# Kernel optimization log

Measured on AMD Instinct MI355X. Metric: run time of the kernel, lower is better.

## Reference

```python
import jax, jax.numpy as jnp
import numpy as np

GROUPS = 32
EPS = 1e-5
HEADS = 8
HEAD_DIM = 40
INNER = HEADS * HEAD_DIM  # 320
QUERY_DIM = 320
CONTEXT_DIM = 768


def setup_inputs() -> dict:
    key = jax.random.key(0)
    ks = jax.random.split(key, 9)
    B, C, H, W = 16, QUERY_DIM, 64, 64
    Lc = 77
    x = jax.random.normal(ks[0], (B, C, H, W), dtype=jnp.float32)
    context = jax.random.normal(ks[1], (B, Lc, CONTEXT_DIM), dtype=jnp.float32)
    # Linear weights in torch layout (out_features, in_features), no bias for q/k/v
    Wq = jax.random.normal(ks[2], (INNER, QUERY_DIM), dtype=jnp.float32) * (QUERY_DIM ** -0.5)
    Wk = jax.random.normal(ks[3], (INNER, CONTEXT_DIM), dtype=jnp.float32) * (CONTEXT_DIM ** -0.5)
    Wv = jax.random.normal(ks[4], (INNER, CONTEXT_DIM), dtype=jnp.float32) * (CONTEXT_DIM ** -0.5)
    Wo = jax.random.normal(ks[5], (QUERY_DIM, INNER), dtype=jnp.float32) * (INNER ** -0.5)
    bo = jnp.zeros((QUERY_DIM,), dtype=jnp.float32)
    gn_scale = jnp.ones((QUERY_DIM,), dtype=jnp.float32)
    gn_bias = jnp.zeros((QUERY_DIM,), dtype=jnp.float32)
    return {"x": x, "context": context, "Wq": Wq, "Wk": Wk, "Wv": Wv,
            "Wo": Wo, "bo": bo, "gn_scale": gn_scale, "gn_bias": gn_bias}


def _group_norm(x, scale, bias):
    # x: [B, C, H, W]
    B, C, H, W = x.shape
    xg = x.reshape(B, GROUPS, C // GROUPS, H, W)
    mean = jnp.mean(xg, axis=(2, 3, 4), keepdims=True)
    var = jnp.var(xg, axis=(2, 3, 4), keepdims=True)
    xn = ((xg - mean) * jax.lax.rsqrt(var + EPS)).reshape(B, C, H, W)
    return xn * scale[None, :, None, None] + bias[None, :, None, None]


def reference(x, context, Wq, Wk, Wv, Wo, bo, gn_scale, gn_bias):
    B, C, H, W = x.shape
    residual = x
    xn = _group_norm(x, gn_scale, gn_bias)
    # (B, C, H, W) -> (B, H*W, C)
    tokens = xn.reshape(B, C, H * W).transpose(0, 2, 1)
    S = H * W
    Lc = context.shape[1]
    scale = HEAD_DIM ** -0.5
    # projections (Linear: x @ W.T); split heads -> [B, h, S, d]
    q = jnp.einsum('bsc,ec->bse', tokens, Wq).reshape(B, S, HEADS, HEAD_DIM).transpose(0, 2, 1, 3)
    k = jnp.einsum('blc,ec->ble', context, Wk).reshape(B, Lc, HEADS, HEAD_DIM).transpose(0, 2, 1, 3)
    v = jnp.einsum('blc,ec->ble', context, Wv).reshape(B, Lc, HEADS, HEAD_DIM).transpose(0, 2, 1, 3)
    scores = jnp.einsum('bhsd,bhkd->bhsk', q, k) * scale  # [B, h, S, Lc]
    attn = jax.nn.softmax(scores, axis=-1)
    out = jnp.einsum('bhsk,bhkd->bhsd', attn, v)  # [B, h, S, d]
    out = out.transpose(0, 2, 1, 3).reshape(B, S, INNER)
    out = jnp.einsum('bse,ce->bsc', out, Wo) + bo  # to_out (dropout is identity at eval)
    out = out.transpose(0, 2, 1).reshape(B, C, H, W)
    return out + residual
```

## Files before the change

### kernel.cpp

```cpp
#include <hip/hip_runtime.h>
#include <hip/hip_bf16.h>
#include <stdint.h>

#define B_    16
#define C_    320
#define S_    4096
#define G_    32
#define LC    77
#define CTX   768
#define HEADS 8
#define HD    40

typedef __bf16 bf16x8_t __attribute__((ext_vector_type(8)));
typedef float  f32x4_t  __attribute__((ext_vector_type(4)));

__device__ __forceinline__ unsigned short f2bf(float f) {
    union { float f; unsigned int u; } v; v.f = f;
    unsigned int r = v.u + 0x7fffu + ((v.u >> 16) & 1u);
    return (unsigned short)(r >> 16);
}
__device__ __forceinline__ float bf2f(unsigned short h) {
    union { unsigned int u; float f; } v; v.u = ((unsigned int)h) << 16;
    return v.f;
}

__device__ __forceinline__ void gload16(const void* g, void* l) {
    __builtin_amdgcn_global_load_lds(
        (const __attribute__((address_space(1))) unsigned int*)g,
        (__attribute__((address_space(3))) unsigned int*)l, 16, 0, 0);
}

__global__ __launch_bounds__(256) void gn_stats(const float* __restrict__ x,
                                                float2* __restrict__ mr) {
    int bg = blockIdx.x;
    const float4* p = (const float4*)(x + (size_t)bg * 40960);
    float s = 0.f, s2 = 0.f;
    for (int i = threadIdx.x; i < 10240; i += 256) {
        float4 v = p[i];
        s  += v.x + v.y + v.z + v.w;
        s2 += v.x * v.x + v.y * v.y + v.z * v.z + v.w * v.w;
    }
    for (int o = 32; o; o >>= 1) {
        s  += __shfl_down(s, o);
        s2 += __shfl_down(s2, o);
    }
    __shared__ float2 red[4];
    int lane = threadIdx.x & 63, wid = threadIdx.x >> 6;
    if (lane == 0) red[wid] = make_float2(s, s2);
    __syncthreads();
    if (threadIdx.x == 0) {
        float a = 0.f, c = 0.f;
        for (int i = 0; i < 4; i++) { a += red[i].x; c += red[i].y; }
        float mean = a / 40960.f;
        float var  = c / 40960.f - mean * mean;
        mr[bg] = make_float2(mean, rsqrtf(var + 1e-5f));
    }
}

__global__ __launch_bounds__(256) void castw(const float* __restrict__ s,
                                             unsigned short* __restrict__ d) {
    int i = blockIdx.x * 256 + threadIdx.x;
    float4 v = ((const float4*)s)[i];
    ushort4 o;
    o.x = f2bf(v.x); o.y = f2bf(v.y); o.z = f2bf(v.z); o.w = f2bf(v.w);
    ((ushort4*)d)[i] = o;
}

__global__ __launch_bounds__(256) void norm_tr(const float* __restrict__ x,
                                               const float2* __restrict__ mr,
                                               const float* __restrict__ gns,
                                               const float* __restrict__ gnb,
                                               unsigned short* __restrict__ tok) {
    int s0 = blockIdx.x * 32, c0 = blockIdx.y * 32, b = blockIdx.z;
    __shared__ unsigned short t[32][33];
    int tx = threadIdx.x & 31, ty = threadIdx.x >> 5;
    #pragma unroll
    for (int i = 0; i < 4; i++) {
        int cl = i * 8 + ty;
        int c = c0 + cl;
        float2 m = mr[b * 32 + c / 10];
        float v = x[((size_t)(b * 320 + c)) * 4096 + s0 + tx];
        v = (v - m.x) * m.y * gns[c] + gnb[c];
        t[cl][tx] = f2bf(v);
    }
    __syncthreads();
    #pragma unroll
    for (int i = 0; i < 4; i++) {
        int sl = i * 8 + ty;
        tok[((size_t)b * 4096 + s0 + sl) * 320 + c0 + tx] = t[tx][sl];
    }
}

__global__ __launch_bounds__(256) void ukern(const float* __restrict__ Wk,
                                             const float* __restrict__ Wq,
                                             unsigned short* __restrict__ Ut) {
    int c = blockIdx.x, h = blockIdx.y;
    int t = threadIdx.x;
    float a0 = 0.f, a1 = 0.f, a2 = 0.f;
    for (int d = 0; d < HD; d++) {
        float wq = Wq[(size_t)(h * HD + d) * 320 + c];
        const float* wkr = Wk + (size_t)(h * HD + d) * CTX;
        a0 += wq * wkr[t];
        a1 += wq * wkr[t + 256];
        a2 += wq * wkr[t + 512];
    }
    unsigned short* o = Ut + ((size_t)h * 320 + c) * CTX;
    o[t]       = f2bf(a0);
    o[t + 256] = f2bf(a1);
    o[t + 512] = f2bf(a2);
}

__global__ __launch_bounds__(256) void kvM_gemm(const float* __restrict__ ctx,
                                                const float* __restrict__ Wv,
                                                const unsigned short* __restrict__ Ut,
                                                unsigned short* __restrict__ vout,
                                                unsigned short* __restrict__ Mout) {
    __shared__ unsigned short la[64][32], lb[64][32];
    int bm = blockIdx.x, bn = blockIdx.y;
    int tid = threadIdx.x, lane = tid & 63, wid = tid >> 6;
    int wm = wid >> 1, wn = wid & 1;
    int lr = tid >> 2, lc = (tid & 3) * 8;
    int fr = lane & 15, kk = (lane >> 4) * 8;

    int arow = bm * 64 + lr; if (arow > 1231) arow = 1231;
    const float* ap = ctx + (size_t)arow * CTX;
    bool isV = (bn < 5);
    const float* wp = isV ? (Wv + (size_t)(bn * 64 + lr) * CTX) : nullptr;
    const unsigned short* up = isV ? nullptr
        : (Ut + ((size_t)((bn - 5) / 5) * 320 + (size_t)((bn - 5) % 5) * 64 + lr) * CTX);

    f32x4_t acc[2][2] = {};
    for (int k0 = 0; k0 < CTX; k0 += 32) {
        float4 a4 = *(const float4*)&ap[k0 + lc];
        float4 a5 = *(const float4*)&ap[k0 + lc + 4];
        ushort4 pa0 = { f2bf(a4.x), f2bf(a4.y), f2bf(a4.z), f2bf(a4.w) };
        ushort4 pa1 = { f2bf(a5.x), f2bf(a5.y), f2bf(a5.z), f2bf(a5.w) };
        *(ushort4*)&la[lr][lc]     = pa0;
        *(ushort4*)&la[lr][lc + 4] = pa1;
        if (isV) {
            float4 w4 = *(const float4*)&wp[k0 + lc];
            float4 w5 = *(const float4*)&wp[k0 + lc + 4];
            ushort4 pw0 = { f2bf(w4.x), f2bf(w4.y), f2bf(w4.z), f2bf(w4.w) };
            ushort4 pw1 = { f2bf(w5.x), f2bf(w5.y), f2bf(w5.z), f2bf(w5.w) };
            *(ushort4*)&lb[lr][lc]     = pw0;
            *(ushort4*)&lb[lr][lc + 4] = pw1;
        } else {
            *(uint4*)&lb[lr][lc] = *(const uint4*)&up[k0 + lc];
        }
        __syncthreads();
        bf16x8_t a0 = *(const bf16x8_t*)&la[wm * 32 + fr][kk];
        bf16x8_t a1 = *(const bf16x8_t*)&la[wm * 32 + 16 + fr][kk];
        bf16x8_t b0 = *(const bf16x8_t*)&lb[wn * 32 + fr][kk];
        bf16x8_t b1 = *(const bf16x8_t*)&lb[wn * 32 + 16 + fr][kk];
        acc[0][0] = __builtin_amdgcn_mfma_f32_16x16x32_bf16(a0, b0, acc[0][0], 0, 0, 0);
        acc[0][1] = __builtin_amdgcn_mfma_f32_16x16x32_bf16(a0, b1, acc[0][1], 0, 0, 0);
        acc[1][0] = __builtin_amdgcn_mfma_f32_16x16x32_bf16(a1, b0, acc[1][0], 0, 0, 0);
        acc[1][1] = __builtin_amdgcn_mfma_f32_16x16x32_bf16(a1, b1, acc[1][1], 0, 0, 0);
        __syncthreads();
    }
    int rg = (lane >> 4) * 4;
    #pragma unroll
    for (int mf = 0; mf < 2; mf++)
        #pragma unroll
        for (int nf = 0; nf < 2; nf++)
            #pragma unroll
            for (int r = 0; r < 4; r++) {
                int row = bm * 64 + wm * 32 + mf * 16 + rg + r;
                if (row < 1232) {
                    int coloff = wn * 32 + nf * 16 + fr;
                    unsigned short val = f2bf(acc[mf][nf][r]);
                    if (isV) {
                        vout[(size_t)row * 320 + bn * 64 + coloff] = val;
                    } else {
                        int bb = row / 77, kv = row - bb * 77;
                        int hh = (bn - 5) / 5;
                        int c = ((bn - 5) % 5) * 64 + coloff;
                        size_t tile = ((size_t)bb * 8 + hh) * 25600;
                        int idx16 = kv * 40 + (c >> 3);
                        int swz = idx16 ^ (kv & 7);
                        Mout[tile + (size_t)swz * 8 + (c & 7)] = val;
                    }
                }
            }
}

__global__ __launch_bounds__(256, 2) void attn8(const unsigned short* __restrict__ tok,
                                                const unsigned short* __restrict__ M,
                                                const unsigned short* __restrict__ v,
                                                unsigned short* __restrict__ att) {
    __shared__ unsigned short Msr[25600];
    unsigned short (*Ps)[104] = (unsigned short (*)[104])Msr;
    unsigned short (*Vt)[104] = (unsigned short (*)[104])(Msr + 13312);

    int tid = threadIdx.x;
    int qt = blockIdx.x, b = blockIdx.y, h0 = blockIdx.z * 4;
    int q0 = qt * 128;
    int lane = tid & 63, wv = tid >> 6;
    int fr = lane & 15, fg = lane >> 4;
    const float scale = 0.15811388300841898f;

    {
        const unsigned short* Mt = M + ((size_t)b * 8 + h0) * 25600;
        #pragma unroll
        for (int i = 0; i < 13; i++) {
            int u = i * 256 + tid;
            if (u < 3200) gload16(Mt + (size_t)u * 8, &Msr[u * 8]);
        }
    }
    uint4 vreg0, vreg1;
    {
        int kv = tid % 77, sg = tid / 77;
        vreg0 = *(const uint4*)&v[((size_t)(b * LC + kv)) * 320 + h0 * HD + sg * 8];
        int idx = tid + 256;
        if (idx < 385) {
            kv = idx % 77; sg = idx / 77;
            vreg1 = *(const uint4*)&v[((size_t)(b * LC + kv)) * 320 + h0 * HD + sg * 8];
        }
    }
    bf16x8_t atok[2][10];
    const size_t tokbase = ((size_t)b * S_ + q0) * 320;
    #pragma unroll
    for (int mf = 0; mf < 2; mf++)
        #pragma unroll
        for (int k = 0; k < 10; k++)
            atok[mf][k] = *(const bf16x8_t*)&tok[tokbase + (size_t)(wv * 32 + mf * 16 + fr) * 320 + k * 32 + fg * 8];

    __syncthreads();

    for (int i = 0; i < 4; i++) {
        int h = h0 + i;

        f32x4_t sc[2][5] = {};
        __builtin_amdgcn_s_setprio(1);
        #pragma unroll
        for (int k = 0; k < 10; k++) {
            bf16x8_t bb[5];
            #pragma unroll
            for (int nf = 0; nf < 5; nf++) {
                int idx16 = (nf * 16 + fr) * 40 + k * 4 + fg;
                bb[nf] = *(const bf16x8_t*)&Msr[(size_t)(idx16 ^ (fr & 7)) * 8];
            }
            #pragma unroll
            for (int mf = 0; mf < 2; mf++)
                #pragma unroll
                for (int nf = 0; nf < 5; nf++)
                    sc[mf][nf] = __builtin_amdgcn_mfma_f32_16x16x32_bf16(atok[mf][k], bb[nf], sc[mf][nf], 0, 0, 0);
        }
        __builtin_amdgcn_s_setprio(0);
        __syncthreads();

        {
            unsigned short e[8];
            int kv = tid % 77, sg = tid / 77;
            *(uint4*)e = vreg0;
            #pragma unroll
            for (int j = 0; j < 8; j++) Vt[sg * 8 + j][kv] = e[j];
            int idx = tid + 256;
            if (idx < 385) {
                kv = idx % 77; sg = idx / 77;
                *(uint4*)e = vreg1;
                #pragma unroll
                for (int j = 0; j < 8; j++) Vt[sg * 8 + j][kv] = e[j];
            }
        }

        {
            uint4 z = {0, 0, 0, 0};
            int zr = wv * 32 + (lane >> 1);
            *(uint4*)((char*)&Ps[zr][80] + (lane & 1) * 16) = z;
        }

        float sm[2][4];
        #pragma unroll
        for (int mf = 0; mf < 2; mf++)
            #pragma unroll
            for (int r = 0; r < 4; r++) {
                float s = 0.f;
                #pragma unroll
                for (int nf = 0; nf < 5; nf++) {
                    float p = (nf < 4 || fr < 13) ? __expf(sc[mf][nf][r] * scale) : 0.f;
                    sc[mf][nf][r] = p;
                    s += p;
                }
                sm[mf][r] = s;
            }
        #pragma unroll
        for (int off = 1; off < 16; off <<= 1)
            #pragma unroll
            for (int mf = 0; mf < 2; mf++)
                #pragma unroll
                for (int r = 0; r < 4; r++)
                    sm[mf][r] += __shfl_xor(sm[mf][r], off);

        #pragma unroll
        for (int mf = 0; mf < 2; mf++)
            #pragma unroll
            for (int nf = 0; nf < 5; nf++)
                #pragma unroll
                for (int r = 0; r < 4; r++)
                    Ps[wv * 32 + mf * 16 + fg * 4 + r][nf * 16 + fr] = f2bf(sc[mf][nf][r]);

        __syncthreads();

        f32x4_t ov[2][3] = {};
        __builtin_amdgcn_s_setprio(1);
        #pragma unroll
        for (int ks = 0; ks < 3; ks++) {
            bf16x8_t vb[3];
            #pragma unroll
            for (int nf = 0; nf < 3; nf++)
                vb[nf] = *(const bf16x8_t*)&Vt[nf * 16 + fr][ks * 32 + fg * 8];
            #pragma unroll
            for (int mf = 0; mf < 2; mf++) {
                bf16x8_t pa = *(const bf16x8_t*)&Ps[wv * 32 + mf * 16 + fr][ks * 32 + fg * 8];
                #pragma unroll
                for (int nf = 0; nf < 3; nf++)
                    ov[mf][nf] = __builtin_amdgcn_mfma_f32_16x16x32_bf16(pa, vb[nf], ov[mf][nf], 0, 0, 0);
            }
        }
        __builtin_amdgcn_s_setprio(0);
        __syncthreads();

        if (i < 3) {
            const unsigned short* Mn = M + ((size_t)b * 8 + h + 1) * 25600;
            #pragma unroll
            for (int j = 0; j < 13; j++) {
                int u = j * 256 + tid;
                if (u < 3200) gload16(Mn + (size_t)u * 8, &Msr[u * 8]);
            }
            int kv = tid % 77, sg = tid / 77;
            vreg0 = *(const uint4*)&v[((size_t)(b * LC + kv)) * 320 + (h + 1) * HD + sg * 8];
            int idx = tid + 256;
            if (idx < 385) {
                kv = idx % 77; sg = idx / 77;
                vreg1 = *(const uint4*)&v[((size_t)(b * LC + kv)) * 320 + (h + 1) * HD + sg * 8];
            }
        }

        #pragma unroll
        for (int mf = 0; mf < 2; mf++) {
            float inv[4];
            #pragma unroll
            for (int r = 0; r < 4; r++) inv[r] = 1.f / sm[mf][r];
            #pragma unroll
            for (int nf = 0; nf < 3; nf++) {
                int d = nf * 16 + fr;
                if (d < HD) {
                    #pragma unroll
                    for (int r = 0; r < 4; r++) {
                        int qrow = q0 + wv * 32 + mf * 16 + fg * 4 + r;
                        att[((size_t)(b * 8 + h) * S_ + qrow) * 40 + d] = f2bf(ov[mf][nf][r] * inv[r]);
                    }
                }
            }
        }
        if (i < 3) __syncthreads();
    }
}

__global__ __launch_bounds__(256) void gemm_oproj2(const unsigned short* __restrict__ att,
                                                   const unsigned short* __restrict__ wo,
                                                   const float* __restrict__ bo,
                                                   const float* __restrict__ resid,
                                                   float* __restrict__ out) {
    __shared__ unsigned short lw[320 * 40];
    __shared__ unsigned short la[64 * 40];
    int tid = threadIdx.x, lane = tid & 63, wv = tid >> 6;
    int fr = lane & 15, fg = lane >> 4;
    int bm = blockIdx.x, b = blockIdx.y;
    int s0 = bm * 64;

    f32x4_t acc[5][4] = {};

    for (int k0 = 0; k0 < 320; k0 += 32) {
        #pragma unroll
        for (int i = 0; i < 7; i++) {
            int u = i * 256 + tid;
            if (u < 1600) {
                int row = u / 5, ch = u % 5;
                int c = ch < 4 ? ch : 0;
                gload16(wo + (size_t)row * 320 + k0 + c * 8, &lw[(size_t)u * 8]);
            }
        }
        {
            int u = tid;
            int row = u / 5, ch = u % 5;
            int c = ch < 4 ? ch : 0;
            int e0 = k0 + c * 8;
            gload16(att + ((size_t)(b * 8 + e0 / 40) * S_ + s0 + row) * 40 + e0 % 40,
                    &la[(size_t)u * 8]);
            u = tid + 256;
            if (u < 320) {
                row = u / 5; ch = u % 5; c = ch < 4 ? ch : 0;
                e0 = k0 + c * 8;
                gload16(att + ((size_t)(b * 8 + e0 / 40) * S_ + s0 + row) * 40 + e0 % 40,
                        &la[(size_t)u * 8]);
            }
        }
        __syncthreads();
        bf16x8_t bfrag[4];
        #pragma unroll
        for (int sf = 0; sf < 4; sf++)
            bfrag[sf] = *(const bf16x8_t*)&la[(sf * 16 + fr) * 40 + fg * 8];
        #pragma unroll
        for (int nf = 0; nf < 5; nf++) {
            bf16x8_t afrag = *(const bf16x8_t*)&lw[(wv * 80 + nf * 16 + fr) * 40 + fg * 8];
            #pragma unroll
            for (int sf = 0; sf < 4; sf++)
                acc[nf][sf] = __builtin_amdgcn_mfma_f32_16x16x32_bf16(afrag, bfrag[sf], acc[nf][sf], 0, 0, 0);
        }
        __syncthreads();
    }

    int nbase = wv * 80;
    #pragma unroll
    for (int nf = 0; nf < 5; nf++) {
        #pragma unroll
        for (int r = 0; r < 4; r++) {
            int n = nbase + nf * 16 + fg * 4 + r;
            float bov = bo[n];
            size_t rowb = ((size_t)(b * 320 + n)) * 4096 + s0;
            #pragma unroll
            for (int sf = 0; sf < 4; sf++) {
                int s = sf * 16 + fr;
                out[rowb + s] = acc[nf][sf][r] + bov + resid[rowb + s];
            }
        }
    }
}

extern "C" void kernel_launch(void* const* d_in, const int* in_sizes, int n_in,
                              void* d_out, int out_size, void* d_ws, size_t ws_size,
                              hipStream_t stream) {
    const float* x    = (const float*)d_in[0];
    const float* ctx  = (const float*)d_in[1];
    const float* Wq   = (const float*)d_in[2];
    const float* Wk   = (const float*)d_in[3];
    const float* Wv   = (const float*)d_in[4];
    const float* Wo   = (const float*)d_in[5];
    const float* bo   = (const float*)d_in[6];
    const float* gns  = (const float*)d_in[7];
    const float* gnb  = (const float*)d_in[8];
    float* out = (float*)d_out;

    char* ws = (char*)d_ws;
    float2*         mr    = (float2*)(ws + 0);
    unsigned short* wo_bf = (unsigned short*)(ws + 4096);
    unsigned short* v_bf  = (unsigned short*)(ws + 208896);
    unsigned short* Mbuf  = (unsigned short*)(ws + 997376);
    unsigned short* tok   = (unsigned short*)(ws + 7550976);
    unsigned short* att   = (unsigned short*)(ws + 49494016);
    unsigned short* Ut    = att;

    gn_stats<<<512, 256, 0, stream>>>(x, mr);
    castw<<<100, 256, 0, stream>>>(Wo, wo_bf);
    ukern<<<dim3(320, 8), 256, 0, stream>>>(Wk, Wq, Ut);
    kvM_gemm<<<dim3(20, 45), 256, 0, stream>>>(ctx, Wv, Ut, v_bf, Mbuf);
    norm_tr<<<dim3(128, 10, 16), 256, 0, stream>>>(x, mr, gns, gnb, tok);
    attn8<<<dim3(32, 16, 2), 256, 0, stream>>>(tok, Mbuf, v_bf, att);
    gemm_oproj2<<<dim3(64, 16), 256, 0, stream>>>(att, wo_bf, bo, x, out);
}
```

Baseline: 185.0 us.

## Split per-head M tile load into two phases to shrink attention LDS footprint

The attention kernel no longer keeps the whole 80-row K-side tile of M in LDS. It prefetches only the first 48 rows and computes those score fragments. It then loads the remaining 32 rows into the freed region, synchronizes, and computes the last two fragments. Shared memory drops from about 51 KB to about 37 KB so more workgroups can share a CU, but the second load is not prefetched, so its latency sits on the critical path and each head iteration gains extra barriers.

```diff
diff --git a/kernel.cpp b/kernel.cpp
--- a/kernel.cpp
+++ b/kernel.cpp
@@ -184,11 +184,11 @@
             }
 }
 
-__global__ __launch_bounds__(256, 2) void attn8(const unsigned short* __restrict__ tok,
+__global__ __launch_bounds__(256, 2) void attn9(const unsigned short* __restrict__ tok,
                                                 const unsigned short* __restrict__ M,
                                                 const unsigned short* __restrict__ v,
                                                 unsigned short* __restrict__ att) {
-    __shared__ unsigned short Msr[25600];
+    __shared__ unsigned short Msr[18304];
     unsigned short (*Ps)[104] = (unsigned short (*)[104])Msr;
     unsigned short (*Vt)[104] = (unsigned short (*)[104])(Msr + 13312);
 
@@ -202,9 +202,17 @@
     {
         const unsigned short* Mt = M + ((size_t)b * 8 + h0) * 25600;
         #pragma unroll
-        for (int i = 0; i < 13; i++) {
+        for (int i = 0; i < 8; i++) {
             int u = i * 256 + tid;
-            if (u < 3200) gload16(Mt + (size_t)u * 8, &Msr[u * 8]);
+            if (u < 1920) gload16(Mt + (size_t)u * 8, &Msr[u * 8]);
+        }
+    }
+    {
+        uint4 z = {0, 0, 0, 0};
+        uint4* zp = (uint4*)&Msr[15360];
+        if (tid < 256) {
+            zp[tid] = z;
+            if (tid + 256 < 368 + 256 && tid < 112) zp[256 + tid] = z;
         }
     }
     uint4 vreg0, vreg1;
@@ -229,26 +237,34 @@
 
     for (int i = 0; i < 4; i++) {
         int h = h0 + i;
-
         f32x4_t sc[2][5] = {};
+
         __builtin_amdgcn_s_setprio(1);
         #pragma unroll
         for (int k = 0; k < 10; k++) {
-            bf16x8_t bb[5];
-            #pragma unroll
-            for (int nf = 0; nf < 5; nf++) {
+            bf16x8_t bb[3];
+            #pragma unroll
+            for (int nf = 0; nf < 3; nf++) {
                 int idx16 = (nf * 16 + fr) * 40 + k * 4 + fg;
                 bb[nf] = *(const bf16x8_t*)&Msr[(size_t)(idx16 ^ (fr & 7)) * 8];
             }
             #pragma unroll
             for (int mf = 0; mf < 2; mf++)
                 #pragma unroll
-                for (int nf = 0; nf < 5; nf++)
+                for (int nf = 0; nf < 3; nf++)
                     sc[mf][nf] = __builtin_amdgcn_mfma_f32_16x16x32_bf16(atok[mf][k], bb[nf], sc[mf][nf], 0, 0, 0);
         }
         __builtin_amdgcn_s_setprio(0);
         __syncthreads();
 
+        {
+            const unsigned short* Mh = M + ((size_t)b * 8 + h) * 25600;
+            #pragma unroll
+            for (int j = 0; j < 5; j++) {
+                int u = j * 256 + tid;
+                gload16(Mh + (size_t)(1920 + u) * 8, &Msr[u * 8]);
+            }
+        }
         {
             unsigned short e[8];
             int kv = tid % 77, sg = tid / 77;
@@ -263,6 +279,26 @@
                 for (int j = 0; j < 8; j++) Vt[sg * 8 + j][kv] = e[j];
             }
         }
+        __syncthreads();
+
+        __builtin_amdgcn_s_setprio(1);
+        #pragma unroll
+        for (int k = 0; k < 10; k++) {
+            bf16x8_t bb[2];
+            #pragma unroll
+            for (int nf2 = 0; nf2 < 2; nf2++) {
+                int idx16 = ((3 + nf2) * 16 + fr) * 40 + k * 4 + fg;
+                int lds16 = (idx16 ^ (fr & 7)) - 1920;
+                bb[nf2] = *(const bf16x8_t*)&Msr[(size_t)lds16 * 8];
+            }
+            #pragma unroll
+            for (int mf = 0; mf < 2; mf++)
+                #pragma unroll
+                for (int nf2 = 0; nf2 < 2; nf2++)
+                    sc[mf][3 + nf2] = __builtin_amdgcn_mfma_f32_16x16x32_bf16(atok[mf][k], bb[nf2], sc[mf][3 + nf2], 0, 0, 0);
+        }
+        __builtin_amdgcn_s_setprio(0);
+        __syncthreads();
 
         {
             uint4 z = {0, 0, 0, 0};
@@ -324,9 +360,9 @@
         if (i < 3) {
             const unsigned short* Mn = M + ((size_t)b * 8 + h + 1) * 25600;
             #pragma unroll
-            for (int j = 0; j < 13; j++) {
+            for (int j = 0; j < 8; j++) {
                 int u = j * 256 + tid;
-                if (u < 3200) gload16(Mn + (size_t)u * 8, &Msr[u * 8]);
+                if (u < 1920) gload16(Mn + (size_t)u * 8, &Msr[u * 8]);
             }
             int kv = tid % 77, sg = tid / 77;
             vreg0 = *(const uint4*)&v[((size_t)(b * LC + kv)) * 320 + (h + 1) * HD + sg * 8];
@@ -457,6 +493,6 @@
     ukern<<<dim3(320, 8), 256, 0, stream>>>(Wk, Wq, Ut);
     kvM_gemm<<<dim3(20, 45), 256, 0, stream>>>(ctx, Wv, Ut, v_bf, Mbuf);
     norm_tr<<<dim3(128, 10, 16), 256, 0, stream>>>(x, mr, gns, gnb, tok);
-    attn8<<<dim3(32, 16, 2), 256, 0, stream>>>(tok, Mbuf, v_bf, att);
+    attn9<<<dim3(32, 16, 2), 256, 0, stream>>>(tok, Mbuf, v_bf, att);
     gemm_oproj2<<<dim3(64, 16), 256, 0, stream>>>(att, wo_bf, bo, x, out);
 }
```

After: 185.1 us. No clear change (+0.1%).
